# Optimization experiments

Hardware: AMD Instinct MI355X
Metric: run time of the kernel (lower is better)

Reference implementation:

```python
import jax, jax.numpy as jnp
import numpy as np


def _tree_constants(depth):
    num_leaves = 2 ** depth
    idx = np.zeros((num_leaves, depth), dtype=np.int32)
    is_right = np.zeros((num_leaves, depth), dtype=np.float32)
    for leaf in range(num_leaves):
        node = 0
        for d in range(depth):
            bit = (leaf >> (depth - 1 - d)) & 1
            idx[leaf, d] = node
            is_right[leaf, d] = float(bit)
            node = 2 * node + 1 + bit
    return jnp.asarray(idx), jnp.asarray(is_right)


def setup_inputs() -> dict:
    key = jax.random.key(0)
    k1, k2, k3 = jax.random.split(key, 3)
    B, D = 8192, 1024
    depth, num_actions = 10, 64
    num_internal = 2 ** depth - 1
    num_leaves = 2 ** depth
    features = jax.random.normal(k1, (B, D), dtype=jnp.float32)
    W = jax.random.normal(k2, (D, num_internal), dtype=jnp.float32) * 0.02
    b = jnp.zeros((num_internal,), dtype=jnp.float32)
    leaf_logits = jax.random.normal(k3, (num_leaves, num_actions), dtype=jnp.float32) * 0.01
    return {"features": features, "W": W, "b": b, "leaf_logits": leaf_logits}


def reference(features, W, b, leaf_logits):
    num_leaves = leaf_logits.shape[0]
    depth = int(np.log2(num_leaves))
    leaf_node_indices, leaf_is_right = _tree_constants(depth)  # [L, depth]

    scores = features @ W + b               # [B, num_internal]
    p_right = jax.nn.sigmoid(scores)         # [B, num_internal]
    g = p_right[:, leaf_node_indices]        # [B, L, depth] gather over internal nodes
    # bit*p_right + (1-bit)*p_left, with p_left = 1 - p_right
    path_probs = leaf_is_right[None] * g + (1.0 - leaf_is_right[None]) * (1.0 - g)
    leaf_prob = jnp.prod(path_probs, axis=2)  # [B, L]
    logits = jnp.einsum('bl,la->ba', leaf_prob, leaf_logits)  # [B, num_actions]
    return logits
```

## Files before the change

### kernel.cpp

```cpp
#include <hip/hip_runtime.h>
#include <cstdint>

typedef __attribute__((ext_vector_type(8))) _Float16 f16x8;
typedef __attribute__((ext_vector_type(4))) float f32x4;

union H2 { uint32_t u; _Float16 h[2]; };

__device__ __forceinline__ void gl_lds16(const void* g, void* lds) {
  __builtin_amdgcn_global_load_lds(
      (const __attribute__((address_space(1))) char*)g,
      (__attribute__((address_space(3))) char*)lds,
      16, 0, 0);
}

__device__ __forceinline__ float hp(uint32_t u, int bit) {
  H2 w; w.u = u; return (float)(bit ? w.h[0] : w.h[1]);
}

__global__ __launch_bounds__(256) void k_convf(const float* __restrict__ in,
                                               _Float16* __restrict__ out) {
  size_t i = ((size_t)blockIdx.x * 256 + threadIdx.x) * 8;
  float4 a = *(const float4*)(in + i);
  float4 b = *(const float4*)(in + i + 4);
  f16x8 o;
  o[0] = (_Float16)a.x; o[1] = (_Float16)a.y; o[2] = (_Float16)a.z; o[3] = (_Float16)a.w;
  o[4] = (_Float16)b.x; o[5] = (_Float16)b.y; o[6] = (_Float16)b.z; o[7] = (_Float16)b.w;
  *(f16x8*)(out + i) = o;
}

__global__ __launch_bounds__(256) void k_convwll(const float* __restrict__ W,
                                                 const float* __restrict__ LL,
                                                 _Float16* __restrict__ Wt,
                                                 _Float16* __restrict__ LLt) {
  __shared__ float tile[64][65];
  int bid = blockIdx.x;
  if (bid < 256) {
    int bx = bid & 15;
    int by = bid >> 4;
    int n0 = bx * 64, k0 = by * 64;
    int tx = threadIdx.x & 63, ty = threadIdx.x >> 6;
#pragma unroll
    for (int r = 0; r < 16; ++r) {
      int kl = ty * 16 + r;
      int n = n0 + tx;
      tile[kl][tx] = (n < 1023) ? W[(size_t)(k0 + kl) * 1023 + n] : 0.0f;
    }
    __syncthreads();
#pragma unroll
    for (int r = 0; r < 16; ++r) {
      int nl = ty * 16 + r;
      Wt[(size_t)(n0 + nl) * 1024 + k0 + tx] = (_Float16)tile[tx][nl];
    }
  } else {
    int a = bid - 256;
    int t = threadIdx.x;
#pragma unroll
    for (int j = 0; j < 4; ++j) {
      int l = t + j * 256;
      LLt[(size_t)a * 1024 + l] = (_Float16)LL[(size_t)l * 64 + a];
    }
  }
}

__global__ __launch_bounds__(256) void k_gemm1(
    const _Float16* __restrict__ fA,
    const _Float16* __restrict__ Wt,
    const float* __restrict__ bv,
    uint32_t* __restrict__ pq)
{
  __shared__ __align__(16) unsigned char As[32768];
  __shared__ __align__(16) unsigned char Bs[32768];
  const int bid = blockIdx.x;
  const int id = (bid & 7) * 64 + (bid >> 3);
  const int mt = id >> 3, nt = id & 7;
  const int m0 = mt * 128, n0 = nt * 128;
  const int tid = threadIdx.x;
  const int wid = tid >> 6, lane = tid & 63;
  const int wm = wid >> 1, wn = wid & 1;
  const int lr = lane & 15, lh = lane >> 4;

  f32x4 acc[4][4];
  for (int i = 0; i < 4; ++i)
    for (int j = 0; j < 4; ++j)
      acc[i][j] = (f32x4)(0.0f);

  const _Float16* srcA[4]; const _Float16* srcB[4];
  int off[4];
#pragma unroll
  for (int j = 0; j < 4; ++j) {
    int blk = j * 4 + wid;
    int q = blk * 64 + lane;
    int i = q >> 3, c = q & 7;
    int cs = c ^ (i & 7);
    srcA[j] = fA + (size_t)(m0 + i) * 1024 + cs * 8;
    srcB[j] = Wt + (size_t)(n0 + i) * 1024 + cs * 8;
    off[j] = blk * 1024;
  }
  const int slot0 = ((0 + lh) ^ (lr & 7)) * 16;
  const int slot1 = ((4 + lh) ^ (lr & 7)) * 16;

#pragma unroll
  for (int j = 0; j < 4; ++j) gl_lds16(srcA[j], As + off[j]);
#pragma unroll
  for (int j = 0; j < 4; ++j) gl_lds16(srcB[j], Bs + off[j]);
  __syncthreads();

  int cb = 0;
  for (int kt = 0; kt < 16; ++kt) {
    if (kt < 15) {
      const int nb = cb ^ 16384;
#pragma unroll
      for (int j = 0; j < 4; ++j) gl_lds16(srcA[j] + (kt + 1) * 64, As + nb + off[j]);
#pragma unroll
      for (int j = 0; j < 4; ++j) gl_lds16(srcB[j] + (kt + 1) * 64, Bs + nb + off[j]);
    }
    __builtin_amdgcn_s_setprio(1);
#pragma unroll
    for (int ph = 0; ph < 2; ++ph) {
      const int sb = (ph ? slot1 : slot0) + cb;
      f16x8 af[4], bf[4];
#pragma unroll
      for (int mf = 0; mf < 4; ++mf)
        af[mf] = *(const f16x8*)(As + (wm * 64 + mf * 16 + lr) * 128 + sb);
#pragma unroll
      for (int nf = 0; nf < 4; ++nf)
        bf[nf] = *(const f16x8*)(Bs + (wn * 64 + nf * 16 + lr) * 128 + sb);
#pragma unroll
      for (int mf = 0; mf < 4; ++mf)
#pragma unroll
        for (int nf = 0; nf < 4; ++nf)
          acc[mf][nf] = __builtin_amdgcn_mfma_f32_16x16x32_f16(af[mf], bf[nf], acc[mf][nf], 0, 0, 0);
    }
    __builtin_amdgcn_s_setprio(0);
    __syncthreads();
    cb ^= 16384;
  }

#pragma unroll
  for (int mf = 0; mf < 4; ++mf) {
#pragma unroll
    for (int nf = 0; nf < 4; ++nf) {
      const int gcol = n0 + wn * 64 + nf * 16 + lr;
      const float bb = (gcol < 1023) ? bv[gcol] : 0.0f;
      const int idx = (gcol + 1) & 1023;
#pragma unroll
      for (int r = 0; r < 4; ++r) {
        const int grow = m0 + wm * 64 + mf * 16 + lh * 4 + r;
        const float s = acc[mf][nf][r] + bb;
        const float e = __expf(-s);
        const float pr = 1.0f / (1.0f + e);
        const float qr = pr * e;
        H2 w; w.h[0] = (_Float16)pr; w.h[1] = (_Float16)qr;
        pq[(size_t)grow * 1024 + idx] = w.u;
      }
    }
  }
}

__global__ __launch_bounds__(256) void k_leaf(const uint32_t* __restrict__ pq,
                                              _Float16* __restrict__ lp) {
  const int tid = threadIdx.x;
  const int s = blockIdx.x * 4 + (tid >> 6);
  const int g = tid & 63;
  const uint32_t* pr = pq + (size_t)s * 1024;

  float P = 1.0f;
  int node = 1;
#pragma unroll
  for (int d = 0; d < 6; ++d) {
    int bit = (g >> (5 - d)) & 1;
    P *= hp(pr[node], bit);
    node = 2 * node + bit;
  }

  const uint32_t u6 = pr[64 + g];
  const uint2 u7 = *(const uint2*)(pr + 128 + 2 * g);
  const uint4 u8 = *(const uint4*)(pr + 256 + 4 * g);
  const uint4 u9a = *(const uint4*)(pr + 512 + 8 * g);
  const uint4 u9b = *(const uint4*)(pr + 512 + 8 * g + 4);

  float c67[2][2];
#pragma unroll
  for (int b6 = 0; b6 < 2; ++b6) {
    const float f6 = hp(u6, b6);
    const uint32_t w7 = b6 ? u7.y : u7.x;
#pragma unroll
    for (int b7 = 0; b7 < 2; ++b7)
      c67[b6][b7] = P * f6 * hp(w7, b7);
  }
  const uint32_t u8a[4] = {u8.x, u8.y, u8.z, u8.w};
  float f8[4][2];
#pragma unroll
  for (int m = 0; m < 4; ++m) { f8[m][0] = hp(u8a[m], 0); f8[m][1] = hp(u8a[m], 1); }
  const uint32_t u9[8] = {u9a.x, u9a.y, u9a.z, u9a.w, u9b.x, u9b.y, u9b.z, u9b.w};
  float f9[8][2];
#pragma unroll
  for (int m = 0; m < 8; ++m) { f9[m][0] = hp(u9[m], 0); f9[m][1] = hp(u9[m], 1); }

  f16x8 o0, o1;
#pragma unroll
  for (int j = 0; j < 16; ++j) {
    float v = c67[j >> 3][(j >> 2) & 1] * f8[j >> 2][(j >> 1) & 1] * f9[j >> 1][j & 1];
    if (j < 8) o0[j] = (_Float16)v; else o1[j - 8] = (_Float16)v;
  }
  *(f16x8*)(lp + (size_t)s * 1024 + g * 16) = o0;
  *(f16x8*)(lp + (size_t)s * 1024 + g * 16 + 8) = o1;
}

__global__ __launch_bounds__(256) void k_gemm2(
    const _Float16* __restrict__ lp,
    const _Float16* __restrict__ LLt,
    float* __restrict__ out)
{
  __shared__ __align__(16) unsigned char As[8192];
  __shared__ __align__(16) unsigned char Bs[8192];
  const int m0 = blockIdx.x * 64;
  const int tid = threadIdx.x;
  const int wid = tid >> 6, lane = tid & 63;
  const int lr = lane & 15, lh = lane >> 4;

  f32x4 acc[4];
  for (int i = 0; i < 4; ++i) acc[i] = (f32x4)(0.0f);

  const _Float16* srcA[2]; const _Float16* srcB[2];
  unsigned char *dstA[2], *dstB[2];
#pragma unroll
  for (int j = 0; j < 2; ++j) {
    int blk = j * 4 + wid;
    int q = blk * 64 + lane;
    int i = q >> 3, c = q & 7;
    int cs = c ^ (i & 7);
    srcA[j] = lp + (size_t)(m0 + i) * 1024 + cs * 8;
    srcB[j] = LLt + (size_t)i * 1024 + cs * 8;
    dstA[j] = As + blk * 1024;
    dstB[j] = Bs + blk * 1024;
  }
  const int slot0 = ((0 + lh) ^ (lr & 7)) * 16;
  const int slot1 = ((4 + lh) ^ (lr & 7)) * 16;

  for (int kt = 0; kt < 16; ++kt) {
    __syncthreads();
#pragma unroll
    for (int j = 0; j < 2; ++j) gl_lds16(srcA[j] + kt * 64, dstA[j]);
#pragma unroll
    for (int j = 0; j < 2; ++j) gl_lds16(srcB[j] + kt * 64, dstB[j]);
    __syncthreads();
#pragma unroll
    for (int ph = 0; ph < 2; ++ph) {
      const int sb = ph ? slot1 : slot0;
      f16x8 af = *(const f16x8*)(As + (wid * 16 + lr) * 128 + sb);
#pragma unroll
      for (int nf = 0; nf < 4; ++nf) {
        f16x8 bf = *(const f16x8*)(Bs + (nf * 16 + lr) * 128 + sb);
        acc[nf] = __builtin_amdgcn_mfma_f32_16x16x32_f16(af, bf, acc[nf], 0, 0, 0);
      }
    }
  }
#pragma unroll
  for (int nf = 0; nf < 4; ++nf)
#pragma unroll
    for (int r = 0; r < 4; ++r) {
      int grow = m0 + wid * 16 + lh * 4 + r;
      int gcol = nf * 16 + lr;
      out[(size_t)grow * 64 + gcol] = acc[nf][r];
    }
}

extern "C" void kernel_launch(void* const* d_in, const int* in_sizes, int n_in,
                              void* d_out, int out_size, void* d_ws, size_t ws_size,
                              hipStream_t stream) {
  const float* feat = (const float*)d_in[0];
  const float* W    = (const float*)d_in[1];
  const float* bv   = (const float*)d_in[2];
  const float* LL   = (const float*)d_in[3];
  float* out = (float*)d_out;
  char* ws = (char*)d_ws;

  _Float16* fA  = (_Float16*)(ws);
  _Float16* Wt  = (_Float16*)(ws + (size_t)(16u << 20));
  _Float16* LLt = (_Float16*)(ws + (size_t)(18u << 20));
  uint32_t* pq  = (uint32_t*)(ws + (size_t)(19u << 20));
  _Float16* lp  = fA;

  k_convf  <<<4096, 256, 0, stream>>>(feat, fA);
  k_convwll<<<320,  256, 0, stream>>>(W, LL, Wt, LLt);
  k_gemm1  <<<512,  256, 0, stream>>>(fA, Wt, bv, pq);
  k_leaf   <<<2048, 256, 0, stream>>>(pq, lp);
  k_gemm2  <<<128,  256, 0, stream>>>(lp, LLt, out);
}
```

Measured before the change: 133.8 us.

## Fuse leaf-probability expansion into second GEMM and merge prep kernels

Merges the features conversion and the W/leaf-logit transpose kernels into one launch, removing a launch boundary. It also fuses leaf-probability computation with the output GEMM. Each block now builds 16 rows of leaf probabilities directly in swizzled LDS and runs the MFMA against double-buffered leaf-logit tiles, so the lp intermediate is never written to or read from global memory. The cost is a 48KB LDS footprint per block and smaller 16-row tiles, under which each block reloads all of LLt.

Measured after the change: 124.7 us. -6.8%, faster.

```diff
diff --git a/kernel.cpp b/kernel.cpp
--- a/kernel.cpp
+++ b/kernel.cpp
@@ -17,26 +17,26 @@
   H2 w; w.u = u; return (float)(bit ? w.h[0] : w.h[1]);
 }
 
-__global__ __launch_bounds__(256) void k_convf(const float* __restrict__ in,
-                                               _Float16* __restrict__ out) {
-  size_t i = ((size_t)blockIdx.x * 256 + threadIdx.x) * 8;
-  float4 a = *(const float4*)(in + i);
-  float4 b = *(const float4*)(in + i + 4);
-  f16x8 o;
-  o[0] = (_Float16)a.x; o[1] = (_Float16)a.y; o[2] = (_Float16)a.z; o[3] = (_Float16)a.w;
-  o[4] = (_Float16)b.x; o[5] = (_Float16)b.y; o[6] = (_Float16)b.z; o[7] = (_Float16)b.w;
-  *(f16x8*)(out + i) = o;
-}
-
-__global__ __launch_bounds__(256) void k_convwll(const float* __restrict__ W,
-                                                 const float* __restrict__ LL,
-                                                 _Float16* __restrict__ Wt,
-                                                 _Float16* __restrict__ LLt) {
+__global__ __launch_bounds__(256) void k_prep(const float* __restrict__ in,
+                                              const float* __restrict__ W,
+                                              const float* __restrict__ LL,
+                                              _Float16* __restrict__ fA,
+                                              _Float16* __restrict__ Wt,
+                                              _Float16* __restrict__ LLt) {
   __shared__ float tile[64][65];
-  int bid = blockIdx.x;
-  if (bid < 256) {
-    int bx = bid & 15;
-    int by = bid >> 4;
+  const int bid = blockIdx.x;
+  if (bid < 4096) {
+    size_t i = ((size_t)bid * 256 + threadIdx.x) * 8;
+    float4 a = *(const float4*)(in + i);
+    float4 b = *(const float4*)(in + i + 4);
+    f16x8 o;
+    o[0] = (_Float16)a.x; o[1] = (_Float16)a.y; o[2] = (_Float16)a.z; o[3] = (_Float16)a.w;
+    o[4] = (_Float16)b.x; o[5] = (_Float16)b.y; o[6] = (_Float16)b.z; o[7] = (_Float16)b.w;
+    *(f16x8*)(fA + i) = o;
+  } else if (bid < 4352) {
+    int b = bid - 4096;
+    int bx = b & 15;
+    int by = b >> 4;
     int n0 = bx * 64, k0 = by * 64;
     int tx = threadIdx.x & 63, ty = threadIdx.x >> 6;
 #pragma unroll
@@ -52,7 +52,7 @@
       Wt[(size_t)(n0 + nl) * 1024 + k0 + tx] = (_Float16)tile[tx][nl];
     }
   } else {
-    int a = bid - 256;
+    int a = bid - 4352;
     int t = threadIdx.x;
 #pragma unroll
     for (int j = 0; j < 4; ++j) {
@@ -157,113 +157,103 @@
   }
 }
 
-__global__ __launch_bounds__(256) void k_leaf(const uint32_t* __restrict__ pq,
-                                              _Float16* __restrict__ lp) {
-  const int tid = threadIdx.x;
-  const int s = blockIdx.x * 4 + (tid >> 6);
-  const int g = tid & 63;
-  const uint32_t* pr = pq + (size_t)s * 1024;
-
-  float P = 1.0f;
-  int node = 1;
-#pragma unroll
-  for (int d = 0; d < 6; ++d) {
-    int bit = (g >> (5 - d)) & 1;
-    P *= hp(pr[node], bit);
-    node = 2 * node + bit;
-  }
-
-  const uint32_t u6 = pr[64 + g];
-  const uint2 u7 = *(const uint2*)(pr + 128 + 2 * g);
-  const uint4 u8 = *(const uint4*)(pr + 256 + 4 * g);
-  const uint4 u9a = *(const uint4*)(pr + 512 + 8 * g);
-  const uint4 u9b = *(const uint4*)(pr + 512 + 8 * g + 4);
-
-  float c67[2][2];
-#pragma unroll
-  for (int b6 = 0; b6 < 2; ++b6) {
-    const float f6 = hp(u6, b6);
-    const uint32_t w7 = b6 ? u7.y : u7.x;
-#pragma unroll
-    for (int b7 = 0; b7 < 2; ++b7)
-      c67[b6][b7] = P * f6 * hp(w7, b7);
-  }
-  const uint32_t u8a[4] = {u8.x, u8.y, u8.z, u8.w};
-  float f8[4][2];
-#pragma unroll
-  for (int m = 0; m < 4; ++m) { f8[m][0] = hp(u8a[m], 0); f8[m][1] = hp(u8a[m], 1); }
-  const uint32_t u9[8] = {u9a.x, u9a.y, u9a.z, u9a.w, u9b.x, u9b.y, u9b.z, u9b.w};
-  float f9[8][2];
-#pragma unroll
-  for (int m = 0; m < 8; ++m) { f9[m][0] = hp(u9[m], 0); f9[m][1] = hp(u9[m], 1); }
-
-  f16x8 o0, o1;
-#pragma unroll
-  for (int j = 0; j < 16; ++j) {
-    float v = c67[j >> 3][(j >> 2) & 1] * f8[j >> 2][(j >> 1) & 1] * f9[j >> 1][j & 1];
-    if (j < 8) o0[j] = (_Float16)v; else o1[j - 8] = (_Float16)v;
-  }
-  *(f16x8*)(lp + (size_t)s * 1024 + g * 16) = o0;
-  *(f16x8*)(lp + (size_t)s * 1024 + g * 16 + 8) = o1;
-}
-
-__global__ __launch_bounds__(256) void k_gemm2(
-    const _Float16* __restrict__ lp,
+__global__ __launch_bounds__(256) void k_out(
+    const uint32_t* __restrict__ pq,
     const _Float16* __restrict__ LLt,
     float* __restrict__ out)
 {
-  __shared__ __align__(16) unsigned char As[8192];
-  __shared__ __align__(16) unsigned char Bs[8192];
-  const int m0 = blockIdx.x * 64;
+  __shared__ __align__(16) unsigned char LP[32768];
+  __shared__ __align__(16) unsigned char Bs[16384];
+  const int m0 = blockIdx.x * 16;
   const int tid = threadIdx.x;
   const int wid = tid >> 6, lane = tid & 63;
   const int lr = lane & 15, lh = lane >> 4;
 
-  f32x4 acc[4];
-  for (int i = 0; i < 4; ++i) acc[i] = (f32x4)(0.0f);
-
-  const _Float16* srcA[2]; const _Float16* srcB[2];
-  unsigned char *dstA[2], *dstB[2];
+#pragma unroll
+  for (int r4 = 0; r4 < 4; ++r4) {
+    const int sl = r4 * 4 + wid;
+    const int g = lane;
+    const uint32_t* pr = pq + (size_t)(m0 + sl) * 1024;
+
+    float P = 1.0f;
+    int node = 1;
+#pragma unroll
+    for (int d = 0; d < 6; ++d) {
+      int bit = (g >> (5 - d)) & 1;
+      P *= hp(pr[node], bit);
+      node = 2 * node + bit;
+    }
+    const uint32_t u6 = pr[64 + g];
+    const uint2 u7 = *(const uint2*)(pr + 128 + 2 * g);
+    const uint4 u8 = *(const uint4*)(pr + 256 + 4 * g);
+    const uint4 u9a = *(const uint4*)(pr + 512 + 8 * g);
+    const uint4 u9b = *(const uint4*)(pr + 512 + 8 * g + 4);
+
+    float c67[2][2];
+#pragma unroll
+    for (int b6 = 0; b6 < 2; ++b6) {
+      const float f6 = hp(u6, b6);
+      const uint32_t w7 = b6 ? u7.y : u7.x;
+#pragma unroll
+      for (int b7 = 0; b7 < 2; ++b7)
+        c67[b6][b7] = P * f6 * hp(w7, b7);
+    }
+    const uint32_t u8a[4] = {u8.x, u8.y, u8.z, u8.w};
+    float f8[4][2];
+#pragma unroll
+    for (int m = 0; m < 4; ++m) { f8[m][0] = hp(u8a[m], 0); f8[m][1] = hp(u8a[m], 1); }
+    const uint32_t u9[8] = {u9a.x, u9a.y, u9a.z, u9a.w, u9b.x, u9b.y, u9b.z, u9b.w};
+    float f9[8][2];
+#pragma unroll
+    for (int m = 0; m < 8; ++m) { f9[m][0] = hp(u9[m], 0); f9[m][1] = hp(u9[m], 1); }
+
+    f16x8 o0, o1;
+#pragma unroll
+    for (int j = 0; j < 16; ++j) {
+      float v = c67[j >> 3][(j >> 2) & 1] * f8[j >> 2][(j >> 1) & 1] * f9[j >> 1][j & 1];
+      if (j < 8) o0[j] = (_Float16)v; else o1[j - 8] = (_Float16)v;
+    }
+    const int key = sl & 7;
+    const int c0 = 2 * g, c1 = 2 * g + 1;
+    *(f16x8*)(LP + sl * 2048 + ((c0 & ~7) | ((c0 & 7) ^ key)) * 16) = o0;
+    *(f16x8*)(LP + sl * 2048 + ((c1 & ~7) | ((c1 & 7) ^ key)) * 16) = o1;
+  }
+
+  const _Float16* srcB[2];
+  int offB[2];
 #pragma unroll
   for (int j = 0; j < 2; ++j) {
     int blk = j * 4 + wid;
     int q = blk * 64 + lane;
     int i = q >> 3, c = q & 7;
-    int cs = c ^ (i & 7);
-    srcA[j] = lp + (size_t)(m0 + i) * 1024 + cs * 8;
-    srcB[j] = LLt + (size_t)i * 1024 + cs * 8;
-    dstA[j] = As + blk * 1024;
-    dstB[j] = Bs + blk * 1024;
-  }
-  const int slot0 = ((0 + lh) ^ (lr & 7)) * 16;
-  const int slot1 = ((4 + lh) ^ (lr & 7)) * 16;
-
+    srcB[j] = LLt + (size_t)i * 1024 + (c ^ (i & 7)) * 8;
+    offB[j] = blk * 1024;
+  }
+#pragma unroll
+  for (int j = 0; j < 2; ++j) gl_lds16(srcB[j], Bs + offB[j]);
+  __syncthreads();
+
+  f32x4 acc = (f32x4)(0.0f);
+  int cb = 0;
   for (int kt = 0; kt < 16; ++kt) {
+    if (kt < 15) {
+      const int nb = cb ^ 8192;
+#pragma unroll
+      for (int j = 0; j < 2; ++j) gl_lds16(srcB[j] + (kt + 1) * 64, Bs + nb + offB[j]);
+    }
+#pragma unroll
+    for (int ph = 0; ph < 2; ++ph) {
+      const int sc = ((ph * 4 + lh) ^ (lr & 7)) * 16;
+      f16x8 af = *(const f16x8*)(LP + lr * 2048 + kt * 128 + sc);
+      f16x8 bf = *(const f16x8*)(Bs + cb + (wid * 16 + lr) * 128 + sc);
+      acc = __builtin_amdgcn_mfma_f32_16x16x32_f16(af, bf, acc, 0, 0, 0);
+    }
     __syncthreads();
-#pragma unroll
-    for (int j = 0; j < 2; ++j) gl_lds16(srcA[j] + kt * 64, dstA[j]);
-#pragma unroll
-    for (int j = 0; j < 2; ++j) gl_lds16(srcB[j] + kt * 64, dstB[j]);
-    __syncthreads();
-#pragma unroll
-    for (int ph = 0; ph < 2; ++ph) {
-      const int sb = ph ? slot1 : slot0;
-      f16x8 af = *(const f16x8*)(As + (wid * 16 + lr) * 128 + sb);
-#pragma unroll
-      for (int nf = 0; nf < 4; ++nf) {
-        f16x8 bf = *(const f16x8*)(Bs + (nf * 16 + lr) * 128 + sb);
-        acc[nf] = __builtin_amdgcn_mfma_f32_16x16x32_f16(af, bf, acc[nf], 0, 0, 0);
-      }
-    }
-  }
-#pragma unroll
-  for (int nf = 0; nf < 4; ++nf)
-#pragma unroll
-    for (int r = 0; r < 4; ++r) {
-      int grow = m0 + wid * 16 + lh * 4 + r;
-      int gcol = nf * 16 + lr;
-      out[(size_t)grow * 64 + gcol] = acc[nf][r];
-    }
+    cb ^= 8192;
+  }
+#pragma unroll
+  for (int r = 0; r < 4; ++r)
+    out[(size_t)(m0 + lh * 4 + r) * 64 + wid * 16 + lr] = acc[r];
 }
 
 extern "C" void kernel_launch(void* const* d_in, const int* in_sizes, int n_in,
@@ -280,11 +270,8 @@
   _Float16* Wt  = (_Float16*)(ws + (size_t)(16u << 20));
   _Float16* LLt = (_Float16*)(ws + (size_t)(18u << 20));
   uint32_t* pq  = (uint32_t*)(ws + (size_t)(19u << 20));
-  _Float16* lp  = fA;
-
-  k_convf  <<<4096, 256, 0, stream>>>(feat, fA);
-  k_convwll<<<320,  256, 0, stream>>>(W, LL, Wt, LLt);
-  k_gemm1  <<<512,  256, 0, stream>>>(fA, Wt, bv, pq);
-  k_leaf   <<<2048, 256, 0, stream>>>(pq, lp);
-  k_gemm2  <<<128,  256, 0, stream>>>(lp, LLt, out);
-}
+
+  k_prep <<<4416, 256, 0, stream>>>(feat, W, LL, fA, Wt, LLt);
+  k_gemm1<<<512,  256, 0, stream>>>(fA, Wt, bv, pq);
+  k_out  <<<512,  256, 0, stream>>>(pq, LLt, out);
+}
```
